# Optimization experiments

Measured on AMD Instinct MI355X. Metric: run time of the kernel, lower is better.

The kernel has to match this reference:

```python
import jax, jax.numpy as jnp
import numpy as np

NEG_SLOPE = 0.2

def gat_conv(x, src, dst, W, a_src, a_dst, b, n_nodes):
    # x: [N, Fin] -> h: [N, Fout]; edges (src->dst) incl. self-loops
    h = x @ W                                   # [N, Fout]
    as_ = h @ a_src                             # [N] per-node source score
    ad_ = h @ a_dst                             # [N] per-node dest score
    e = jax.nn.leaky_relu(as_[src] + ad_[dst], NEG_SLOPE)   # [E]
    # segment softmax over edges sharing the same destination
    e_max = jax.ops.segment_max(e, dst, num_segments=n_nodes)
    e_exp = jnp.exp(e - e_max[dst])
    e_sum = jax.ops.segment_sum(e_exp, dst, num_segments=n_nodes)
    alpha = e_exp / (e_sum[dst] + 1e-16)        # [E]
    out = jax.ops.segment_sum(alpha[:, None] * h[src], dst, num_segments=n_nodes)
    return out + b

def setup_inputs() -> dict:
    key = jax.random.key(0)
    ks = jax.random.split(key, 12)
    N, E, Fin, H = 100000, 3200000, 128, 32
    def g(k, shape, scale):
        return jax.random.normal(k, shape, dtype=jnp.float32) * scale
    return {
        "x": g(ks[0], (N, Fin), 1.0),
        "edge_index": jax.random.randint(ks[1], (2, E), 0, N, dtype=jnp.int32),
        "W1": g(ks[2], (Fin, H), 1.0 / np.sqrt(Fin)),
        "att_src1": g(ks[3], (H,), 1.0 / np.sqrt(H)),
        "att_dst1": g(ks[4], (H,), 1.0 / np.sqrt(H)),
        "b1": jnp.zeros((H,), jnp.float32),
        "W2": g(ks[5], (H, H), 1.0 / np.sqrt(H)),
        "att_src2": g(ks[6], (H,), 1.0 / np.sqrt(H)),
        "att_dst2": g(ks[7], (H,), 1.0 / np.sqrt(H)),
        "b2": jnp.zeros((H,), jnp.float32),
        "Wf": g(ks[8], (H, H), 1.0 / np.sqrt(H)),
        "bf": jnp.zeros((H,), jnp.float32),
    }

def reference(x, edge_index, W1, att_src1, att_dst1, b1, W2, att_src2, att_dst2, b2, Wf, bf):
    n_nodes = x.shape[0]
    loops = jnp.arange(n_nodes, dtype=edge_index.dtype)
    src = jnp.concatenate([edge_index[0], loops])  # add_self_loops=True (PyG default)
    dst = jnp.concatenate([edge_index[1], loops])
    h = jax.nn.relu(gat_conv(x, src, dst, W1, att_src1, att_dst1, b1, n_nodes))
    h = jax.nn.relu(gat_conv(h, src, dst, W2, att_src2, att_dst2, b2, n_nodes))
    return h @ Wf + bf
```

## Files before the change

kernel.cpp:

```cpp
#include <hip/hip_runtime.h>

#define NEG_SLOPE 0.2f
#define BK_SH 8
#define BK_SZ 256
#define MAXBUCK 512
#define EPB 8192

typedef _Float16 half8 __attribute__((ext_vector_type(8)));
typedef float f32x4 __attribute__((ext_vector_type(4)));

__global__ __launch_bounds__(256) void k_castx(const float* __restrict__ x,
                                               _Float16* __restrict__ xh,
                                               int n8) {
  int i = blockIdx.x * 256 + threadIdx.x;
  if (i >= n8) return;
  const float4* p = reinterpret_cast<const float4*>(x) + 2 * (size_t)i;
  float4 v0 = p[0], v1 = p[1];
  half8 h;
  h[0] = (_Float16)v0.x; h[1] = (_Float16)v0.y;
  h[2] = (_Float16)v0.z; h[3] = (_Float16)v0.w;
  h[4] = (_Float16)v1.x; h[5] = (_Float16)v1.y;
  h[6] = (_Float16)v1.z; h[7] = (_Float16)v1.w;
  *(reinterpret_cast<half8*>(xh) + i) = h;
}

__global__ __launch_bounds__(256) void k_castW(const float* __restrict__ W,
                                               _Float16* __restrict__ Wt) {
  for (int i = threadIdx.x; i < 128 * 32; i += 256) {
    int k = i >> 5, f = i & 31;
    Wt[f * 128 + k] = (_Float16)W[i];
  }
}

__global__ __launch_bounds__(256) void k_feat_mfma(
    const _Float16* __restrict__ xh, const _Float16* __restrict__ Wt,
    const float* __restrict__ a_src, const float* __restrict__ a_dst,
    _Float16* __restrict__ Hh, float* __restrict__ as_, float* __restrict__ ad_,
    int N) {
  int w = threadIdx.x >> 6;
  int lane = threadIdx.x & 63;
  int base = (blockIdx.x * 4 + w) * 16;
  if (base >= N) return;
  int row16 = lane & 15;
  int kg = lane >> 4;
  f32x4 acc0 = {0.f, 0.f, 0.f, 0.f};
  f32x4 acc1 = {0.f, 0.f, 0.f, 0.f};
  const half8* xa =
      reinterpret_cast<const half8*>(xh + (size_t)(base + row16) * 128 + kg * 8);
#pragma unroll
  for (int kt = 0; kt < 4; ++kt) {
    half8 a = xa[kt * 4];
    half8 b0 = *reinterpret_cast<const half8*>(Wt + (size_t)row16 * 128 +
                                               kt * 32 + kg * 8);
    half8 b1 = *reinterpret_cast<const half8*>(Wt + (size_t)(16 + row16) * 128 +
                                               kt * 32 + kg * 8);
    acc0 = __builtin_amdgcn_mfma_f32_16x16x32_f16(a, b0, acc0, 0, 0, 0);
    acc1 = __builtin_amdgcn_mfma_f32_16x16x32_f16(a, b1, acc1, 0, 0, 0);
  }
  float aS0 = a_src[row16], aS1 = a_src[16 + row16];
  float aD0 = a_dst[row16], aD1 = a_dst[16 + row16];
  float tS[4], tD[4];
#pragma unroll
  for (int r = 0; r < 4; ++r) {
    int row = base + kg * 4 + r;
    Hh[(size_t)row * 32 + row16] = (_Float16)acc0[r];
    Hh[(size_t)row * 32 + 16 + row16] = (_Float16)acc1[r];
    tS[r] = acc0[r] * aS0 + acc1[r] * aS1;
    tD[r] = acc0[r] * aD0 + acc1[r] * aD1;
  }
#pragma unroll
  for (int off = 1; off <= 8; off <<= 1) {
#pragma unroll
    for (int r = 0; r < 4; ++r) {
      tS[r] += __shfl_xor(tS[r], off, 64);
      tD[r] += __shfl_xor(tD[r], off, 64);
    }
  }
  if (row16 == 0) {
#pragma unroll
    for (int r = 0; r < 4; ++r) {
      as_[base + kg * 4 + r] = tS[r];
      ad_[base + kg * 4 + r] = tD[r];
    }
  }
}

__global__ __launch_bounds__(256) void k_feat32(
    const float* __restrict__ X, const float* __restrict__ W,
    const float* __restrict__ a_src, const float* __restrict__ a_dst,
    _Float16* __restrict__ Hh, float* __restrict__ as_, float* __restrict__ ad_,
    int N) {
  __shared__ float sW[32 * 32];
  __shared__ float sX[8][32];
  for (int i = threadIdx.x; i < 32 * 32; i += 256) sW[i] = W[i];
  int node0 = blockIdx.x * 8;
  {
    int i = threadIdx.x;
    int n = node0 + (i >> 5);
    sX[i >> 5][i & 31] = (n < N) ? X[(size_t)n * 32 + (i & 31)] : 0.f;
  }
  __syncthreads();
  int g = threadIdx.x >> 5;
  int f = threadIdx.x & 31;
  int n = node0 + g;
  if (n >= N) return;
  float acc = 0.f;
#pragma unroll
  for (int k = 0; k < 32; ++k) acc += sX[g][k] * sW[k * 32 + f];
  Hh[(size_t)n * 32 + f] = (_Float16)acc;
  float vs = acc * a_src[f];
  float vd = acc * a_dst[f];
#pragma unroll
  for (int off = 16; off; off >>= 1) {
    vs += __shfl_down(vs, off, 32);
    vd += __shfl_down(vd, off, 32);
  }
  if (f == 0) {
    as_[n] = vs;
    ad_[n] = vd;
  }
}

__global__ __launch_bounds__(256) void k_zero(int* __restrict__ p, int n) {
  int i = blockIdx.x * 256 + threadIdx.x;
  if (i < n) p[i] = 0;
}

__global__ __launch_bounds__(256) void k_bhist(const int* __restrict__ ei,
                                               int E, int* __restrict__ bcnt,
                                               int nbuck) {
  __shared__ int h[MAXBUCK];
  for (int i = threadIdx.x; i < nbuck; i += 256) h[i] = 0;
  __syncthreads();
  long base = (long)blockIdx.x * EPB;
#pragma unroll 4
  for (int i = 0; i < EPB / 256; ++i) {
    long e = base + i * 256 + threadIdx.x;
    if (e < E) atomicAdd(&h[ei[E + e] >> BK_SH], 1);
  }
  __syncthreads();
  for (int i = threadIdx.x; i < nbuck; i += 256)
    if (h[i]) atomicAdd(&bcnt[i], h[i]);
}

__global__ __launch_bounds__(1024) void k_scan(const int* __restrict__ bcnt,
                                               int* __restrict__ boff,
                                               int* __restrict__ bcur,
                                               int* __restrict__ ptr, int nbuck,
                                               int N, int E) {
  __shared__ int s[1024];
  int t = threadIdx.x;
  int v = (t < nbuck) ? bcnt[t] : 0;
  s[t] = v;
  __syncthreads();
  for (int off = 1; off < 1024; off <<= 1) {
    int x = (t >= off) ? s[t - off] : 0;
    __syncthreads();
    s[t] += x;
    __syncthreads();
  }
  if (t < nbuck) {
    boff[t] = s[t] - v;
    bcur[t] = s[t] - v;
  }
  if (t == 0) {
    boff[nbuck] = E;
    ptr[N] = E;
  }
}

__global__ __launch_bounds__(256) void k_binA(const int* __restrict__ ei, int E,
                                              int* __restrict__ bcur,
                                              unsigned* __restrict__ packed,
                                              int nbuck) {
  __shared__ int h[MAXBUCK];
  __shared__ int lbase[MAXBUCK];
  __shared__ int lb[MAXBUCK];
  __shared__ int cur[MAXBUCK];
  __shared__ int psum[256];
  __shared__ unsigned rec[EPB];
  __shared__ unsigned short bkt[EPB];
  int t = threadIdx.x;
  for (int i = t; i < MAXBUCK; i += 256) h[i] = 0;
  __syncthreads();
  long base = (long)blockIdx.x * EPB;
  int cnt = (int)((E - base) < EPB ? (E - base) : EPB);
#pragma unroll 4
  for (int i = 0; i < EPB / 256; ++i) {
    int e = i * 256 + t;
    if (e < cnt) atomicAdd(&h[ei[E + base + e] >> BK_SH], 1);
  }
  __syncthreads();
  for (int i = t; i < nbuck; i += 256)
    lbase[i] = h[i] ? atomicAdd(&bcur[i], h[i]) : 0;
  int a0 = h[2 * t], a1 = h[2 * t + 1];
  psum[t] = a0 + a1;
  __syncthreads();
  for (int off = 1; off < 256; off <<= 1) {
    int x = (t >= off) ? psum[t - off] : 0;
    __syncthreads();
    psum[t] += x;
    __syncthreads();
  }
  int pex = psum[t] - (a0 + a1);
  lb[2 * t] = pex;
  lb[2 * t + 1] = pex + a0;
  cur[2 * t] = pex;
  cur[2 * t + 1] = pex + a0;
  __syncthreads();
#pragma unroll 4
  for (int i = 0; i < EPB / 256; ++i) {
    int e = i * 256 + t;
    if (e < cnt) {
      int s = ei[base + e], d = ei[E + base + e];
      int b = d >> BK_SH;
      int pos = atomicAdd(&cur[b], 1);
      rec[pos] = ((unsigned)s << 8) | (unsigned)(d & (BK_SZ - 1));
      bkt[pos] = (unsigned short)b;
    }
  }
  __syncthreads();
  for (int i = t; i < cnt; i += 256) {
    int b = bkt[i];
    packed[(size_t)lbase[b] + (i - lb[b])] = rec[i];
  }
}

__global__ __launch_bounds__(256) void k_binB(const unsigned* __restrict__ packed,
                                              const int* __restrict__ boff,
                                              int* __restrict__ ptr,
                                              int* __restrict__ srcs, int N) {
  int b = blockIdx.x;
  int beg = boff[b], end = boff[b + 1];
  int t = threadIdx.x;
  __shared__ int lcnt[BK_SZ];
  __shared__ int sc[BK_SZ];
  __shared__ int lcur[BK_SZ];
  lcnt[t] = 0;
  __syncthreads();
  for (int i = beg + t; i < end; i += 256)
    atomicAdd(&lcnt[packed[i] & (BK_SZ - 1)], 1);
  __syncthreads();
  int v = lcnt[t];
  sc[t] = v;
  __syncthreads();
  for (int off = 1; off < 256; off <<= 1) {
    int x = (t >= off) ? sc[t - off] : 0;
    __syncthreads();
    sc[t] += x;
    __syncthreads();
  }
  int excl = sc[t] - v;
  int node = (b << BK_SH) + t;
  if (node < N) ptr[node] = beg + excl;
  lcur[t] = excl;
  __syncthreads();
  for (int i = beg + t; i < end; i += 256) {
    unsigned p = packed[i];
    int slot = atomicAdd(&lcur[p & (BK_SZ - 1)], 1);
    srcs[(size_t)beg + slot] = (int)(p >> 8);
  }
}

__global__ __launch_bounds__(256) void k_gather(
    const int* __restrict__ ptr, const int* __restrict__ srcs,
    const _Float16* __restrict__ Hh, const float* __restrict__ as_,
    const float* __restrict__ ad_, const float* __restrict__ b,
    float* __restrict__ OUT, int N, int do_relu) {
  int g = threadIdx.x >> 5;
  int lane = threadIdx.x & 31;
  int sub = lane >> 2;
  int q = lane & 3;
  int d = blockIdx.x * 8 + g;
  if (d >= N) return;
  float ad_d = ad_[d];
  float acc[8] = {0.f, 0.f, 0.f, 0.f, 0.f, 0.f, 0.f, 0.f};
  float sumw = 0.f;
  int beg = ptr[d], end = ptr[d + 1];
  for (int j = beg; j < end; j += 8) {
    if (sub < end - j) {
      int sid = srcs[j + sub];
      float sc2 = as_[sid] + ad_d;
      float el = sc2 > 0.f ? sc2 : NEG_SLOPE * sc2;
      float w = __expf(el);
      half8 hv = *reinterpret_cast<const half8*>(Hh + (size_t)sid * 32 + q * 8);
#pragma unroll
      for (int i = 0; i < 8; ++i) acc[i] += w * (float)hv[i];
      sumw += w;
    }
  }
#pragma unroll
  for (int off = 4; off <= 16; off <<= 1) {
#pragma unroll
    for (int i = 0; i < 8; ++i) acc[i] += __shfl_xor(acc[i], off, 32);
    sumw += __shfl_xor(sumw, off, 32);
  }
  if (sub == 0) {
    float s0 = as_[d] + ad_d;
    float e0 = s0 > 0.f ? s0 : NEG_SLOPE * s0;
    float w0 = __expf(e0);
    half8 hs = *reinterpret_cast<const half8*>(Hh + (size_t)d * 32 + q * 8);
#pragma unroll
    for (int i = 0; i < 8; ++i) acc[i] += w0 * (float)hs[i];
    sumw += w0;
    float inv = 1.f / (sumw + 1e-16f);
    float4 o1, o2;
    o1.x = acc[0] * inv + b[q * 8 + 0];
    o1.y = acc[1] * inv + b[q * 8 + 1];
    o1.z = acc[2] * inv + b[q * 8 + 2];
    o1.w = acc[3] * inv + b[q * 8 + 3];
    o2.x = acc[4] * inv + b[q * 8 + 4];
    o2.y = acc[5] * inv + b[q * 8 + 5];
    o2.z = acc[6] * inv + b[q * 8 + 6];
    o2.w = acc[7] * inv + b[q * 8 + 7];
    if (do_relu) {
      o1.x = fmaxf(o1.x, 0.f); o1.y = fmaxf(o1.y, 0.f);
      o1.z = fmaxf(o1.z, 0.f); o1.w = fmaxf(o1.w, 0.f);
      o2.x = fmaxf(o2.x, 0.f); o2.y = fmaxf(o2.y, 0.f);
      o2.z = fmaxf(o2.z, 0.f); o2.w = fmaxf(o2.w, 0.f);
    }
    *reinterpret_cast<float4*>(OUT + (size_t)d * 32 + q * 8) = o1;
    *reinterpret_cast<float4*>(OUT + (size_t)d * 32 + q * 8 + 4) = o2;
  }
}

__global__ __launch_bounds__(256) void k_final(
    const float* __restrict__ X, const float* __restrict__ W,
    const float* __restrict__ b, float* __restrict__ OUT, int N) {
  __shared__ float sW[32 * 32];
  __shared__ float sX[8][32];
  for (int i = threadIdx.x; i < 32 * 32; i += 256) sW[i] = W[i];
  int node0 = blockIdx.x * 8;
  {
    int i = threadIdx.x;
    int n = node0 + (i >> 5);
    sX[i >> 5][i & 31] = (n < N) ? X[(size_t)n * 32 + (i & 31)] : 0.f;
  }
  __syncthreads();
  int g = threadIdx.x >> 5;
  int f = threadIdx.x & 31;
  int n = node0 + g;
  if (n >= N) return;
  float acc = b[f];
#pragma unroll
  for (int k = 0; k < 32; ++k) acc += sX[g][k] * sW[k * 32 + f];
  OUT[(size_t)n * 32 + f] = acc;
}

extern "C" void kernel_launch(void* const* d_in, const int* in_sizes, int n_in,
                              void* d_out, int out_size, void* d_ws,
                              size_t ws_size, hipStream_t stream) {
  const float* x = (const float*)d_in[0];
  const int* ei = (const int*)d_in[1];
  const float* W1 = (const float*)d_in[2];
  const float* as1 = (const float*)d_in[3];
  const float* ad1 = (const float*)d_in[4];
  const float* b1 = (const float*)d_in[5];
  const float* W2 = (const float*)d_in[6];
  const float* as2 = (const float*)d_in[7];
  const float* ad2 = (const float*)d_in[8];
  const float* b2 = (const float*)d_in[9];
  const float* Wf = (const float*)d_in[10];
  const float* bf = (const float*)d_in[11];
  float* out = (float*)d_out;

  const int H = in_sizes[3];
  const int FIN = in_sizes[2] / H;
  const int N = in_sizes[0] / FIN;
  const int E = in_sizes[1] / 2;
  const int nbuck = (N + BK_SZ - 1) >> BK_SH;
  (void)n_in; (void)out_size; (void)ws_size; (void)H;

  size_t r0 = (size_t)E * 4;
  size_t xhB = (size_t)N * FIN * 2;
  size_t bfB = (size_t)N * 32 * 4;
  if (xhB > r0) r0 = xhB;
  if (bfB > r0) r0 = bfB;
  char* basep = (char*)d_ws;
  unsigned* packed = (unsigned*)basep;
  _Float16* xh = (_Float16*)basep;
  float* Bf = (float*)basep;
  char* p = basep + r0;
  _Float16* Hh = (_Float16*)p;  p += (size_t)N * 32 * 2;
  _Float16* Wt = (_Float16*)p;  p += (size_t)128 * 32 * 2;
  float* asv = (float*)p;       p += (size_t)N * 4;
  float* adv = (float*)p;       p += (size_t)N * 4;
  int* ptr = (int*)p;           p += (size_t)(N + 1) * 4;
  int* srcs = (int*)p;          p += (size_t)E * 4;
  int* bcnt = (int*)p;          p += (size_t)nbuck * 4;
  int* boff = (int*)p;          p += (size_t)(nbuck + 1) * 4;
  int* bcur = (int*)p;

  const int nodeBlocks = (N + 7) / 8;
  const int binBlocks = (E + EPB - 1) / EPB;
  const int mfmaBlocks = (N / 16 + 3) / 4;

  k_zero<<<(nbuck + 255) / 256, 256, 0, stream>>>(bcnt, nbuck);
  k_bhist<<<binBlocks, 256, 0, stream>>>(ei, E, bcnt, nbuck);
  k_scan<<<1, 1024, 0, stream>>>(bcnt, boff, bcur, ptr, nbuck, N, E);
  k_binA<<<binBlocks, 256, 0, stream>>>(ei, E, bcur, packed, nbuck);
  k_binB<<<nbuck, 256, 0, stream>>>(packed, boff, ptr, srcs, N);

  k_castx<<<(N * FIN / 8 + 255) / 256, 256, 0, stream>>>(x, xh, N * FIN / 8);
  k_castW<<<1, 256, 0, stream>>>(W1, Wt);
  k_feat_mfma<<<mfmaBlocks, 256, 0, stream>>>(xh, Wt, as1, ad1, Hh, asv, adv, N);
  k_gather<<<nodeBlocks, 256, 0, stream>>>(ptr, srcs, Hh, asv, adv, b1, Bf, N, 1);

  k_feat32<<<nodeBlocks, 256, 0, stream>>>(Bf, W2, as2, ad2, Hh, asv, adv, N);
  k_gather<<<nodeBlocks, 256, 0, stream>>>(ptr, srcs, Hh, asv, adv, b2, Bf, N, 1);

  k_final<<<nodeBlocks, 256, 0, stream>>>(Bf, Wf, bf, out, N);
}
```

Before: 253.1 us.

## Split node features into two 16-wide halves and gather each half separately

Stores the fp16 projected features as two separate N×16 arrays and runs the edge gather twice per layer, once per half, with 16 edges processed in parallel per destination. The aim is to shrink the randomly accessed feature table each pass touches to 3.2MB so it sits better in cache and gets a higher hit rate. In exchange, the edge list, source scores and exp computations are read and evaluated twice per layer, which doubles that index traffic and ALU work.

```diff
diff --git a/kernel.cpp b/kernel.cpp
--- a/kernel.cpp
+++ b/kernel.cpp
@@ -35,8 +35,8 @@
 __global__ __launch_bounds__(256) void k_feat_mfma(
     const _Float16* __restrict__ xh, const _Float16* __restrict__ Wt,
     const float* __restrict__ a_src, const float* __restrict__ a_dst,
-    _Float16* __restrict__ Hh, float* __restrict__ as_, float* __restrict__ ad_,
-    int N) {
+    _Float16* __restrict__ Ht0, _Float16* __restrict__ Ht1,
+    float* __restrict__ as_, float* __restrict__ ad_, int N) {
   int w = threadIdx.x >> 6;
   int lane = threadIdx.x & 63;
   int base = (blockIdx.x * 4 + w) * 16;
@@ -63,8 +63,8 @@
 #pragma unroll
   for (int r = 0; r < 4; ++r) {
     int row = base + kg * 4 + r;
-    Hh[(size_t)row * 32 + row16] = (_Float16)acc0[r];
-    Hh[(size_t)row * 32 + 16 + row16] = (_Float16)acc1[r];
+    Ht0[(size_t)row * 16 + row16] = (_Float16)acc0[r];
+    Ht1[(size_t)row * 16 + row16] = (_Float16)acc1[r];
     tS[r] = acc0[r] * aS0 + acc1[r] * aS1;
     tD[r] = acc0[r] * aD0 + acc1[r] * aD1;
   }
@@ -88,8 +88,8 @@
 __global__ __launch_bounds__(256) void k_feat32(
     const float* __restrict__ X, const float* __restrict__ W,
     const float* __restrict__ a_src, const float* __restrict__ a_dst,
-    _Float16* __restrict__ Hh, float* __restrict__ as_, float* __restrict__ ad_,
-    int N) {
+    _Float16* __restrict__ Ht0, _Float16* __restrict__ Ht1,
+    float* __restrict__ as_, float* __restrict__ ad_, int N) {
   __shared__ float sW[32 * 32];
   __shared__ float sX[8][32];
   for (int i = threadIdx.x; i < 32 * 32; i += 256) sW[i] = W[i];
@@ -107,7 +107,10 @@
   float acc = 0.f;
 #pragma unroll
   for (int k = 0; k < 32; ++k) acc += sX[g][k] * sW[k * 32 + f];
-  Hh[(size_t)n * 32 + f] = (_Float16)acc;
+  if (f < 16)
+    Ht0[(size_t)n * 16 + f] = (_Float16)acc;
+  else
+    Ht1[(size_t)n * 16 + (f - 16)] = (_Float16)acc;
   float vs = acc * a_src[f];
   float vd = acc * a_dst[f];
 #pragma unroll
@@ -262,35 +265,35 @@
   }
 }
 
-__global__ __launch_bounds__(256) void k_gather(
+__global__ __launch_bounds__(256) void k_gather16(
     const int* __restrict__ ptr, const int* __restrict__ srcs,
-    const _Float16* __restrict__ Hh, const float* __restrict__ as_,
+    const _Float16* __restrict__ Ht, const float* __restrict__ as_,
     const float* __restrict__ ad_, const float* __restrict__ b,
-    float* __restrict__ OUT, int N, int do_relu) {
+    float* __restrict__ OUT, int N, int do_relu, int hoff) {
   int g = threadIdx.x >> 5;
   int lane = threadIdx.x & 31;
-  int sub = lane >> 2;
-  int q = lane & 3;
+  int sub = lane >> 1;
+  int q = lane & 1;
   int d = blockIdx.x * 8 + g;
   if (d >= N) return;
   float ad_d = ad_[d];
   float acc[8] = {0.f, 0.f, 0.f, 0.f, 0.f, 0.f, 0.f, 0.f};
   float sumw = 0.f;
   int beg = ptr[d], end = ptr[d + 1];
-  for (int j = beg; j < end; j += 8) {
+  for (int j = beg; j < end; j += 16) {
     if (sub < end - j) {
       int sid = srcs[j + sub];
       float sc2 = as_[sid] + ad_d;
       float el = sc2 > 0.f ? sc2 : NEG_SLOPE * sc2;
       float w = __expf(el);
-      half8 hv = *reinterpret_cast<const half8*>(Hh + (size_t)sid * 32 + q * 8);
+      half8 hv = *reinterpret_cast<const half8*>(Ht + (size_t)sid * 16 + q * 8);
 #pragma unroll
       for (int i = 0; i < 8; ++i) acc[i] += w * (float)hv[i];
       sumw += w;
     }
   }
 #pragma unroll
-  for (int off = 4; off <= 16; off <<= 1) {
+  for (int off = 2; off <= 16; off <<= 1) {
 #pragma unroll
     for (int i = 0; i < 8; ++i) acc[i] += __shfl_xor(acc[i], off, 32);
     sumw += __shfl_xor(sumw, off, 32);
@@ -299,28 +302,29 @@
     float s0 = as_[d] + ad_d;
     float e0 = s0 > 0.f ? s0 : NEG_SLOPE * s0;
     float w0 = __expf(e0);
-    half8 hs = *reinterpret_cast<const half8*>(Hh + (size_t)d * 32 + q * 8);
+    half8 hs = *reinterpret_cast<const half8*>(Ht + (size_t)d * 16 + q * 8);
 #pragma unroll
     for (int i = 0; i < 8; ++i) acc[i] += w0 * (float)hs[i];
     sumw += w0;
     float inv = 1.f / (sumw + 1e-16f);
+    int fb = hoff + q * 8;
     float4 o1, o2;
-    o1.x = acc[0] * inv + b[q * 8 + 0];
-    o1.y = acc[1] * inv + b[q * 8 + 1];
-    o1.z = acc[2] * inv + b[q * 8 + 2];
-    o1.w = acc[3] * inv + b[q * 8 + 3];
-    o2.x = acc[4] * inv + b[q * 8 + 4];
-    o2.y = acc[5] * inv + b[q * 8 + 5];
-    o2.z = acc[6] * inv + b[q * 8 + 6];
-    o2.w = acc[7] * inv + b[q * 8 + 7];
+    o1.x = acc[0] * inv + b[fb + 0];
+    o1.y = acc[1] * inv + b[fb + 1];
+    o1.z = acc[2] * inv + b[fb + 2];
+    o1.w = acc[3] * inv + b[fb + 3];
+    o2.x = acc[4] * inv + b[fb + 4];
+    o2.y = acc[5] * inv + b[fb + 5];
+    o2.z = acc[6] * inv + b[fb + 6];
+    o2.w = acc[7] * inv + b[fb + 7];
     if (do_relu) {
       o1.x = fmaxf(o1.x, 0.f); o1.y = fmaxf(o1.y, 0.f);
       o1.z = fmaxf(o1.z, 0.f); o1.w = fmaxf(o1.w, 0.f);
       o2.x = fmaxf(o2.x, 0.f); o2.y = fmaxf(o2.y, 0.f);
       o2.z = fmaxf(o2.z, 0.f); o2.w = fmaxf(o2.w, 0.f);
     }
-    *reinterpret_cast<float4*>(OUT + (size_t)d * 32 + q * 8) = o1;
-    *reinterpret_cast<float4*>(OUT + (size_t)d * 32 + q * 8 + 4) = o2;
+    *reinterpret_cast<float4*>(OUT + (size_t)d * 32 + fb) = o1;
+    *reinterpret_cast<float4*>(OUT + (size_t)d * 32 + fb + 4) = o2;
   }
 }
 
@@ -381,14 +385,15 @@
   _Float16* xh = (_Float16*)basep;
   float* Bf = (float*)basep;
   char* p = basep + r0;
-  _Float16* Hh = (_Float16*)p;  p += (size_t)N * 32 * 2;
-  _Float16* Wt = (_Float16*)p;  p += (size_t)128 * 32 * 2;
-  float* asv = (float*)p;       p += (size_t)N * 4;
-  float* adv = (float*)p;       p += (size_t)N * 4;
-  int* ptr = (int*)p;           p += (size_t)(N + 1) * 4;
-  int* srcs = (int*)p;          p += (size_t)E * 4;
-  int* bcnt = (int*)p;          p += (size_t)nbuck * 4;
-  int* boff = (int*)p;          p += (size_t)(nbuck + 1) * 4;
+  _Float16* Ht0 = (_Float16*)p;  p += (size_t)N * 16 * 2;
+  _Float16* Ht1 = (_Float16*)p;  p += (size_t)N * 16 * 2;
+  _Float16* Wt = (_Float16*)p;   p += (size_t)128 * 32 * 2;
+  float* asv = (float*)p;        p += (size_t)N * 4;
+  float* adv = (float*)p;        p += (size_t)N * 4;
+  int* ptr = (int*)p;            p += (size_t)(N + 1) * 4;
+  int* srcs = (int*)p;           p += (size_t)E * 4;
+  int* bcnt = (int*)p;           p += (size_t)nbuck * 4;
+  int* boff = (int*)p;           p += (size_t)(nbuck + 1) * 4;
   int* bcur = (int*)p;
 
   const int nodeBlocks = (N + 7) / 8;
@@ -403,11 +408,19 @@
 
   k_castx<<<(N * FIN / 8 + 255) / 256, 256, 0, stream>>>(x, xh, N * FIN / 8);
   k_castW<<<1, 256, 0, stream>>>(W1, Wt);
-  k_feat_mfma<<<mfmaBlocks, 256, 0, stream>>>(xh, Wt, as1, ad1, Hh, asv, adv, N);
-  k_gather<<<nodeBlocks, 256, 0, stream>>>(ptr, srcs, Hh, asv, adv, b1, Bf, N, 1);
-
-  k_feat32<<<nodeBlocks, 256, 0, stream>>>(Bf, W2, as2, ad2, Hh, asv, adv, N);
-  k_gather<<<nodeBlocks, 256, 0, stream>>>(ptr, srcs, Hh, asv, adv, b2, Bf, N, 1);
+  k_feat_mfma<<<mfmaBlocks, 256, 0, stream>>>(xh, Wt, as1, ad1, Ht0, Ht1, asv,
+                                              adv, N);
+  k_gather16<<<nodeBlocks, 256, 0, stream>>>(ptr, srcs, Ht0, asv, adv, b1, Bf,
+                                             N, 1, 0);
+  k_gather16<<<nodeBlocks, 256, 0, stream>>>(ptr, srcs, Ht1, asv, adv, b1, Bf,
+                                             N, 1, 16);
+
+  k_feat32<<<nodeBlocks, 256, 0, stream>>>(Bf, W2, as2, ad2, Ht0, Ht1, asv, adv,
+                                           N);
+  k_gather16<<<nodeBlocks, 256, 0, stream>>>(ptr, srcs, Ht0, asv, adv, b2, Bf,
+                                             N, 1, 0);
+  k_gather16<<<nodeBlocks, 256, 0, stream>>>(ptr, srcs, Ht1, asv, adv, b2, Bf,
+                                             N, 1, 16);
 
   k_final<<<nodeBlocks, 256, 0, stream>>>(Bf, Wf, bf, out, N);
 }
```

Result: slower. 308.3 us (+21.8%).

## Fuse final linear layer into second gather and software-pipeline edge loads

Applied to the files above, without the earlier changes.

The final 32x32 linear projection is folded into the second-layer gather kernel through shared memory, which removes a separate launch and a full write and read of the intermediate node features. The gather loop is also software-pipelined: the next batch of source ids, scores and feature rows is loaded before the current batch is accumulated, to hide gather latency. Out-of-range nodes are clamped rather than returning early so that every thread reaches the barrier. The costs are extra shared memory per block, one extra speculative iteration of loads, and higher register pressure.

```diff
diff --git a/kernel.cpp b/kernel.cpp
--- a/kernel.cpp
+++ b/kernel.cpp
@@ -262,32 +262,46 @@
   }
 }
 
-__global__ __launch_bounds__(256) void k_gather(
+template <int FINAL>
+__global__ __launch_bounds__(256) void k_gatherT(
     const int* __restrict__ ptr, const int* __restrict__ srcs,
     const _Float16* __restrict__ Hh, const float* __restrict__ as_,
     const float* __restrict__ ad_, const float* __restrict__ b,
-    float* __restrict__ OUT, int N, int do_relu) {
+    const float* __restrict__ Wf, const float* __restrict__ bf,
+    float* __restrict__ OUT, int N) {
+  __shared__ float sWf[32 * 32];
+  __shared__ float sO[8][33];
+  if (FINAL) {
+    for (int i = threadIdx.x; i < 32 * 32; i += 256) sWf[i] = Wf[i];
+  }
   int g = threadIdx.x >> 5;
   int lane = threadIdx.x & 31;
   int sub = lane >> 2;
   int q = lane & 3;
   int d = blockIdx.x * 8 + g;
-  if (d >= N) return;
-  float ad_d = ad_[d];
+  int dc = d < N ? d : N - 1;
+  float ad_d = ad_[dc];
   float acc[8] = {0.f, 0.f, 0.f, 0.f, 0.f, 0.f, 0.f, 0.f};
   float sumw = 0.f;
-  int beg = ptr[d], end = ptr[d + 1];
-  for (int j = beg; j < end; j += 8) {
-    if (sub < end - j) {
-      int sid = srcs[j + sub];
-      float sc2 = as_[sid] + ad_d;
-      float el = sc2 > 0.f ? sc2 : NEG_SLOPE * sc2;
-      float w = __expf(el);
-      half8 hv = *reinterpret_cast<const half8*>(Hh + (size_t)sid * 32 + q * 8);
-#pragma unroll
-      for (int i = 0; i < 8; ++i) acc[i] += w * (float)hv[i];
-      sumw += w;
-    }
+  int beg = ptr[dc], end = ptr[dc + 1];
+  int j = beg;
+  bool v0 = sub < end - j;
+  int sid0 = v0 ? srcs[j + sub] : dc;
+  float sa0 = as_[sid0];
+  half8 hv0 = *reinterpret_cast<const half8*>(Hh + (size_t)sid0 * 32 + q * 8);
+  while (j < end) {
+    int jn = j + 8;
+    bool v1 = sub < end - jn;
+    int sid1 = v1 ? srcs[jn + sub] : dc;
+    float sa1 = as_[sid1];
+    half8 hv1 = *reinterpret_cast<const half8*>(Hh + (size_t)sid1 * 32 + q * 8);
+    float sc2 = sa0 + ad_d;
+    float el = sc2 > 0.f ? sc2 : NEG_SLOPE * sc2;
+    float w = v0 ? __expf(el) : 0.f;
+#pragma unroll
+    for (int i = 0; i < 8; ++i) acc[i] += w * (float)hv0[i];
+    sumw += w;
+    j = jn; v0 = v1; sid0 = sid1; sa0 = sa1; hv0 = hv1;
   }
 #pragma unroll
   for (int off = 4; off <= 16; off <<= 1) {
@@ -296,55 +310,36 @@
     sumw += __shfl_xor(sumw, off, 32);
   }
   if (sub == 0) {
-    float s0 = as_[d] + ad_d;
+    float s0 = as_[dc] + ad_d;
     float e0 = s0 > 0.f ? s0 : NEG_SLOPE * s0;
     float w0 = __expf(e0);
-    half8 hs = *reinterpret_cast<const half8*>(Hh + (size_t)d * 32 + q * 8);
+    half8 hs = *reinterpret_cast<const half8*>(Hh + (size_t)dc * 32 + q * 8);
 #pragma unroll
     for (int i = 0; i < 8; ++i) acc[i] += w0 * (float)hs[i];
     sumw += w0;
     float inv = 1.f / (sumw + 1e-16f);
-    float4 o1, o2;
-    o1.x = acc[0] * inv + b[q * 8 + 0];
-    o1.y = acc[1] * inv + b[q * 8 + 1];
-    o1.z = acc[2] * inv + b[q * 8 + 2];
-    o1.w = acc[3] * inv + b[q * 8 + 3];
-    o2.x = acc[4] * inv + b[q * 8 + 4];
-    o2.y = acc[5] * inv + b[q * 8 + 5];
-    o2.z = acc[6] * inv + b[q * 8 + 6];
-    o2.w = acc[7] * inv + b[q * 8 + 7];
-    if (do_relu) {
-      o1.x = fmaxf(o1.x, 0.f); o1.y = fmaxf(o1.y, 0.f);
-      o1.z = fmaxf(o1.z, 0.f); o1.w = fmaxf(o1.w, 0.f);
-      o2.x = fmaxf(o2.x, 0.f); o2.y = fmaxf(o2.y, 0.f);
-      o2.z = fmaxf(o2.z, 0.f); o2.w = fmaxf(o2.w, 0.f);
+    if (FINAL) {
+#pragma unroll
+      for (int i = 0; i < 8; ++i)
+        sO[g][q * 8 + i] = fmaxf(acc[i] * inv + b[q * 8 + i], 0.f);
+    } else if (d < N) {
+      f32x4 o1, o2;
+#pragma unroll
+      for (int i = 0; i < 4; ++i) {
+        o1[i] = fmaxf(acc[i] * inv + b[q * 8 + i], 0.f);
+        o2[i] = fmaxf(acc[4 + i] * inv + b[q * 8 + 4 + i], 0.f);
+      }
+      *reinterpret_cast<f32x4*>(OUT + (size_t)d * 32 + q * 8) = o1;
+      *reinterpret_cast<f32x4*>(OUT + (size_t)d * 32 + q * 8 + 4) = o2;
     }
-    *reinterpret_cast<float4*>(OUT + (size_t)d * 32 + q * 8) = o1;
-    *reinterpret_cast<float4*>(OUT + (size_t)d * 32 + q * 8 + 4) = o2;
-  }
-}
-
-__global__ __launch_bounds__(256) void k_final(
-    const float* __restrict__ X, const float* __restrict__ W,
-    const float* __restrict__ b, float* __restrict__ OUT, int N) {
-  __shared__ float sW[32 * 32];
-  __shared__ float sX[8][32];
-  for (int i = threadIdx.x; i < 32 * 32; i += 256) sW[i] = W[i];
-  int node0 = blockIdx.x * 8;
-  {
-    int i = threadIdx.x;
-    int n = node0 + (i >> 5);
-    sX[i >> 5][i & 31] = (n < N) ? X[(size_t)n * 32 + (i & 31)] : 0.f;
-  }
-  __syncthreads();
-  int g = threadIdx.x >> 5;
-  int f = threadIdx.x & 31;
-  int n = node0 + g;
-  if (n >= N) return;
-  float acc = b[f];
-#pragma unroll
-  for (int k = 0; k < 32; ++k) acc += sX[g][k] * sW[k * 32 + f];
-  OUT[(size_t)n * 32 + f] = acc;
+  }
+  if (FINAL) {
+    __syncthreads();
+    float accf = bf[lane];
+#pragma unroll
+    for (int k = 0; k < 32; ++k) accf += sO[g][k] * sWf[k * 32 + lane];
+    if (d < N) OUT[(size_t)d * 32 + lane] = accf;
+  }
 }
 
 extern "C" void kernel_launch(void* const* d_in, const int* in_sizes, int n_in,
@@ -404,10 +399,10 @@
   k_castx<<<(N * FIN / 8 + 255) / 256, 256, 0, stream>>>(x, xh, N * FIN / 8);
   k_castW<<<1, 256, 0, stream>>>(W1, Wt);
   k_feat_mfma<<<mfmaBlocks, 256, 0, stream>>>(xh, Wt, as1, ad1, Hh, asv, adv, N);
-  k_gather<<<nodeBlocks, 256, 0, stream>>>(ptr, srcs, Hh, asv, adv, b1, Bf, N, 1);
+  k_gatherT<0><<<nodeBlocks, 256, 0, stream>>>(ptr, srcs, Hh, asv, adv, b1,
+                                               nullptr, nullptr, Bf, N);
 
   k_feat32<<<nodeBlocks, 256, 0, stream>>>(Bf, W2, as2, ad2, Hh, asv, adv, N);
-  k_gather<<<nodeBlocks, 256, 0, stream>>>(ptr, srcs, Hh, asv, adv, b2, Bf, N, 1);
-
-  k_final<<<nodeBlocks, 256, 0, stream>>>(Bf, Wf, bf, out, N);
-}
+  k_gatherT<1><<<nodeBlocks, 256, 0, stream>>>(ptr, srcs, Hh, asv, adv, b2, Wf,
+                                               bf, out, N);
+}
```

Result: faster. 236.0 us (-6.7%).
